# Performance work log

Hardware: AMD Instinct MI355X
Metric: run time of the kernel (lower is better)

## Reference

```python
import jax, jax.numpy as jnp
import numpy as np

HIDDEN = 1024
NHEAD = 16
HEAD_DIM = HIDDEN // NHEAD
B, S = 2, 2048


def setup_inputs() -> dict:
    key = jax.random.key(0)
    ks = jax.random.split(key, 10)
    scale = 1.0 / np.sqrt(HIDDEN)
    inp = {
        "x": jax.random.normal(ks[0], (B, S, HIDDEN), dtype=jnp.float32),
        "mask": jax.random.randint(ks[1], (B, S), 0, 2).astype(bool),
        "Wq": jax.random.normal(ks[2], (HIDDEN, HIDDEN), dtype=jnp.float32) * scale,
        "bq": jnp.zeros((HIDDEN,), dtype=jnp.float32),
        "Wk": jax.random.normal(ks[3], (HIDDEN, HIDDEN), dtype=jnp.float32) * scale,
        "bk": jnp.zeros((HIDDEN,), dtype=jnp.float32),
        "Wv": jax.random.normal(ks[4], (HIDDEN, HIDDEN), dtype=jnp.float32) * scale,
        "bv": jnp.zeros((HIDDEN,), dtype=jnp.float32),
        "Wo": jax.random.normal(ks[5], (HIDDEN, HIDDEN), dtype=jnp.float32) * scale,
        "bo": jnp.zeros((HIDDEN,), dtype=jnp.float32),
    }
    return inp


def reference(x, mask, Wq, bq, Wk, bk, Wv, bv, Wo, bo):
    B_, S_, H = x.shape
    # QKV projections (torch Linear: x @ W.T + b), split into heads -> [B, nhead, S, head_dim]
    def split_heads(t):
        return t.reshape(B_, S_, NHEAD, HEAD_DIM).transpose(0, 2, 1, 3)

    q = split_heads(x @ Wq.T + bq)
    k = split_heads(x @ Wk.T + bk)
    v = split_heads(x @ Wv.T + bv)

    # scaled dot-product scores: [B, nhead, S, S]
    energy = jnp.einsum("bhqd,bhkd->bhqk", q, k) / jnp.sqrt(jnp.float32(HEAD_DIM))

    # combined padding + diagonal-exclusion mask: mask keys where mask[b,k] is True,
    # but never mask the diagonal (self) position
    eye = jnp.eye(S_, dtype=bool)  # [S, S]
    attn_mask = mask[:, None, None, :] & ~eye[None, None, :, :]  # [B, 1, S, S] broadcast over heads
    energy = jnp.where(attn_mask, -jnp.inf, energy)

    attention = jax.nn.softmax(energy, axis=-1)
    out = jnp.einsum("bhqk,bhkd->bhqd", attention, v)  # [B, nhead, S, head_dim]
    out = out.transpose(0, 2, 1, 3).reshape(B_, S_, H)
    return out @ Wo.T + bo
```

## Files before the change

### kernel.cpp

```cpp
#include <hip/hip_runtime.h>

typedef __attribute__((ext_vector_type(8))) short short8;
typedef __attribute__((ext_vector_type(4))) float f32x4;
typedef __attribute__((ext_vector_type(16))) float f32x16;
typedef __attribute__((ext_vector_type(4))) unsigned short ushort4v;

#define HIDDEN 1024
#define NHEAD 16
#define HD 64
#define BATCH 2
#define SEQ 2048
#define MROWS (BATCH * SEQ)
#define QSCALE 0.18033688011112042f

__device__ __forceinline__ unsigned short f2b(float f) {
  union { float f; unsigned u; } v; v.f = f;
  unsigned r = v.u + 0x7fffu + ((v.u >> 16) & 1u);
  return (unsigned short)(r >> 16);
}

__device__ __forceinline__ unsigned cvt_pk_bf16(float lo, float hi) {
  unsigned r;
  asm("v_cvt_pk_bf16_f32 %0, %1, %2" : "=v"(r) : "v"(lo), "v"(hi));
  return r;
}

__device__ __forceinline__ float fexp2(float x) {
#if __has_builtin(__builtin_amdgcn_exp2f)
  return __builtin_amdgcn_exp2f(x);
#else
  return exp2f(x);
#endif
}

__device__ __forceinline__ void gll16(const void* g, void* l) {
  __builtin_amdgcn_global_load_lds(
      (__attribute__((address_space(1))) void*)g,
      (__attribute__((address_space(3))) void*)l, 16, 0, 0);
}

__global__ void prep_kernel(const float* __restrict__ x,
                            const float* __restrict__ Wq,
                            const float* __restrict__ Wk,
                            const float* __restrict__ Wv,
                            const float* __restrict__ Wo,
                            unsigned short* __restrict__ xb,
                            unsigned short* __restrict__ wqb,
                            unsigned short* __restrict__ wkb,
                            unsigned short* __restrict__ wvb,
                            unsigned short* __restrict__ wob) {
  int bid = blockIdx.x;
  const float* src;
  unsigned short* dst;
  int base;
  if (bid < 4096)      { src = x;  dst = xb;  base = bid; }
  else if (bid < 5120) { src = Wq; dst = wqb; base = bid - 4096; }
  else if (bid < 6144) { src = Wk; dst = wkb; base = bid - 5120; }
  else if (bid < 7168) { src = Wv; dst = wvb; base = bid - 6144; }
  else                 { src = Wo; dst = wob; base = bid - 7168; }
  int i = (base * 256 + threadIdx.x) * 4;
  float4 v = *reinterpret_cast<const float4*>(src + i);
  ushort4v o;
  o.x = f2b(v.x); o.y = f2b(v.y); o.z = f2b(v.z); o.w = f2b(v.w);
  *reinterpret_cast<ushort4v*>(dst + i) = o;
}

__global__ void amask_kernel(const int* __restrict__ m, float* __restrict__ am,
                             int n) {
  int i = blockIdx.x * blockDim.x + threadIdx.x;
  if (i < n) am[i] = m[i] ? -1e30f : 0.f;
}

template <int MODE>
__global__ __launch_bounds__(256) void gemm128_kernel(
    const unsigned short* __restrict__ A,
    const unsigned short* __restrict__ W0,
    const unsigned short* __restrict__ W1,
    const unsigned short* __restrict__ W2,
    const float* __restrict__ c0, const float* __restrict__ c1,
    const float* __restrict__ c2, void* __restrict__ o0,
    void* __restrict__ o1, void* __restrict__ o2) {
  __shared__ __align__(16) unsigned short Al[2][128 * 64];
  __shared__ __align__(16) unsigned short Bl[2][128 * 64];
  const int t = threadIdx.x;
  const int w = t >> 6, l = t & 63;
  const int hi = l >> 4, lo16 = l & 15;
  const int wr = w >> 1, wc = w & 1;
  const int m0 = blockIdx.x * 128;
  const int n0 = blockIdx.y * 128;
  const int K = HIDDEN;

  const unsigned short* Bsel;
  const float* bias;
  int region = 0, n_loc = n0;
  if (MODE == 0) {
    region = n0 >> 10;
    n_loc = n0 & 1023;
    Bsel = region == 0 ? W0 : (region == 1 ? W1 : W2);
    bias = region == 0 ? c0 : (region == 1 ? c1 : c2);
  } else {
    Bsel = W0;
    bias = c0;
  }

  const int srow = w * 32 + (l >> 3);
  const int schunk = (l & 7) ^ (l >> 3);
  const int rsw = (lo16 & 7);

  const unsigned short* pA[4];
  const unsigned short* pB[4];
#pragma unroll
  for (int i = 0; i < 4; ++i) {
    pA[i] = A + (size_t)(m0 + srow + i * 8) * K + schunk * 8;
    pB[i] = Bsel + (size_t)(n_loc + srow + i * 8) * K + schunk * 8;
  }

  f32x4 acc[4][4];
#pragma unroll
  for (int mi = 0; mi < 4; ++mi)
#pragma unroll
    for (int f = 0; f < 4; ++f) acc[mi][f] = f32x4{0.f, 0.f, 0.f, 0.f};

#pragma unroll
  for (int i = 0; i < 4; ++i) {
    gll16(pA[i], &Al[0][(w * 32 + i * 8) * 64]);
    gll16(pB[i], &Bl[0][(w * 32 + i * 8) * 64]);
    pA[i] += 64; pB[i] += 64;
  }
  __syncthreads();

  auto step = [&](int knext, int BUF) __attribute__((always_inline)) {
    if (knext < K) {
#pragma unroll
      for (int i = 0; i < 4; ++i) {
        gll16(pA[i], &Al[BUF ^ 1][(w * 32 + i * 8) * 64]);
        gll16(pB[i], &Bl[BUF ^ 1][(w * 32 + i * 8) * 64]);
        pA[i] += 64; pB[i] += 64;
      }
    }
#pragma unroll
    for (int kk = 0; kk < 2; ++kk) {
      short8 af[4], bf[4];
#pragma unroll
      for (int mi = 0; mi < 4; ++mi) {
        int row = wr * 64 + mi * 16 + lo16;
        af[mi] = *reinterpret_cast<const short8*>(
            &Al[BUF][row * 64 + (((kk * 4 + hi) ^ rsw) * 8)]);
      }
#pragma unroll
      for (int f = 0; f < 4; ++f) {
        int row = wc * 64 + f * 16 + lo16;
        bf[f] = *reinterpret_cast<const short8*>(
            &Bl[BUF][row * 64 + (((kk * 4 + hi) ^ rsw) * 8)]);
      }
#pragma unroll
      for (int mi = 0; mi < 4; ++mi)
#pragma unroll
        for (int f = 0; f < 4; ++f)
          acc[mi][f] =
              __builtin_amdgcn_mfma_f32_16x16x32_bf16(af[mi], bf[f], acc[mi][f], 0, 0, 0);
    }
    __syncthreads();
  };

  for (int kt = 0; kt < K; kt += 128) {
    step(kt + 64, 0);
    step(kt + 128, 1);
  }

#pragma unroll
  for (int mi = 0; mi < 4; ++mi)
#pragma unroll
    for (int f = 0; f < 4; ++f) {
      int mbase = m0 + wr * 64 + mi * 16 + hi * 4;
      int n_rel = n_loc + wc * 64 + f * 16 + lo16;
      float bv_ = bias[n_rel];
      if (MODE == 0 && region == 2) {
        int b = mbase >> 11, s = mbase & 2047, d = n_rel & 63, h = n_rel >> 6;
        uint2 pk;
        pk.x = cvt_pk_bf16(acc[mi][f][0] + bv_, acc[mi][f][1] + bv_);
        pk.y = cvt_pk_bf16(acc[mi][f][2] + bv_, acc[mi][f][3] + bv_);
        *reinterpret_cast<uint2*>(
            (unsigned short*)o2 + ((size_t)(b * NHEAD + h) * HD + d) * SEQ + s) = pk;
        continue;
      }
#pragma unroll
      for (int j = 0; j < 4; ++j) {
        float v = acc[mi][f][j] + bv_;
        int mm = mbase + j;
        if (MODE == 0) {
          int b = mm >> 11, s = mm & 2047, h = n_rel >> 6, d = n_rel & 63;
          if (region == 0)
            ((unsigned short*)o0)[((size_t)(b * NHEAD + h) * SEQ + s) * HD + d] =
                f2b(v * QSCALE);
          else
            ((unsigned short*)o1)[((size_t)(b * NHEAD + h) * SEQ + s) * HD + d] =
                f2b(v);
        } else {
          ((float*)o0)[(size_t)mm * HIDDEN + n_rel] = v;
        }
      }
    }
}

__global__ __launch_bounds__(512) void attn_kernel(
    const unsigned short* __restrict__ Q, const unsigned short* __restrict__ Km,
    const unsigned short* __restrict__ Vt, const float* __restrict__ amf,
    unsigned short* __restrict__ O) {
  __shared__ __align__(16) unsigned short KV[2][2][64 * 64];
  __shared__ float SrwS[4][64];
  const int t = threadIdx.x;
  const int w = t >> 6, l = t & 63;
  const int q31 = l & 31, hi32 = l >> 5;
  const int qg = w >> 1, half = w & 1;
  const int bh = blockIdx.y;
  const int b = bh >> 4, h = bh & 15;
  const int q0w = blockIdx.x * 128 + qg * 32;
  const int q = q0w + q31;
  const bool diagw = (half == (qg & 1));
  const int dtile = blockIdx.x * 128 + (qg >> 1) * 64;

  const unsigned short* Qb = Q + (size_t)bh * SEQ * HD;
  const unsigned short* Kb = Km + (size_t)bh * SEQ * HD;
  const unsigned short* Vb = Vt + (size_t)bh * HD * SEQ;
  const float* mb = amf + b * SEQ + half * 32;

  short8 qf[4];
#pragma unroll
  for (int dc = 0; dc < 4; ++dc)
    qf[dc] = *reinterpret_cast<const short8*>(
        Qb + (size_t)q * HD + dc * 16 + hi32 * 8);

  f32x16 o0, o1;
#pragma unroll
  for (int r = 0; r < 16; ++r) { o0[r] = 0.f; o1[r] = 0.f; }
  float srw = 0.f;

  const int srow = w * 8 + (l >> 3);
  const int sc_ = ((l & 7) ^ (l >> 3) ^ (w & 3)) * 8;
  const unsigned short* pK = Kb + (size_t)srow * HD + sc_;
  const unsigned short* pV = Vb + (size_t)srow * SEQ + sc_;

  gll16(pK, &KV[0][0][(w * 8) * 64]);
  gll16(pV, &KV[0][1][(w * 8) * 64]);
  pK += 64 * HD; pV += 64;
  __syncthreads();

  const int rk = (q31 & 7) ^ (q31 >> 3);

  auto step = [&](int k0, int BUF) __attribute__((always_inline)) {
    float4 a0[4];
#pragma unroll
    for (int g = 0; g < 4; ++g)
      a0[g] = *reinterpret_cast<const float4*>(mb + k0 + g * 8 + hi32 * 4);

    if (k0 + 64 < SEQ) {
      gll16(pK, &KV[BUF ^ 1][0][(w * 8) * 64]);
      gll16(pV, &KV[BUF ^ 1][1][(w * 8) * 64]);
      pK += 64 * HD; pV += 64;
    }

    f32x16 s0;
    if (diagw && k0 == dtile) {
      int kb = hi32 * 4;
#pragma unroll
      for (int g = 0; g < 4; ++g) {
        if (kb + g * 8 + 0 == q31) a0[g].x = 0.f;
        if (kb + g * 8 + 1 == q31) a0[g].y = 0.f;
        if (kb + g * 8 + 2 == q31) a0[g].z = 0.f;
        if (kb + g * 8 + 3 == q31) a0[g].w = 0.f;
      }
    }
#pragma unroll
    for (int g = 0; g < 4; ++g) {
      s0[4 * g + 0] = a0[g].x; s0[4 * g + 1] = a0[g].y;
      s0[4 * g + 2] = a0[g].z; s0[4 * g + 3] = a0[g].w;
    }

    __builtin_amdgcn_s_setprio(1);
#pragma unroll
    for (int dc = 0; dc < 4; ++dc) {
      short8 kf = *reinterpret_cast<const short8*>(
          &KV[BUF][0][(half * 32 + q31) * 64 + (((dc * 2 + hi32) ^ rk) * 8)]);
      s0 = __builtin_amdgcn_mfma_f32_32x32x16_bf16(kf, qf[dc], s0, 0, 0, 0);
    }
    __builtin_amdgcn_s_setprio(0);

    float sum = 0.f;
#pragma unroll
    for (int r = 0; r < 16; ++r) {
      float p = fexp2(s0[r]);
      s0[r] = p;
      sum += p;
    }
    {
      unsigned a = __float_as_uint(sum), bsw = a;
      auto rr = __builtin_amdgcn_permlane32_swap(a, bsw, false, false);
      sum = __uint_as_float(rr[0]) + __uint_as_float(rr[1]);
    }
    srw += sum;

    unsigned c[8];
#pragma unroll
    for (int R = 0; R < 4; ++R) {
      c[R * 2 + 0] = cvt_pk_bf16(s0[4 * R + 0], s0[4 * R + 1]);
      c[R * 2 + 1] = cvt_pk_bf16(s0[4 * R + 2], s0[4 * R + 3]);
    }

    short8 pb[2];
#pragma unroll
    for (int sl = 0; sl < 2; ++sl) {
      const int R0 = sl * 2;
      auto r0 = __builtin_amdgcn_permlane32_swap(c[R0 * 2 + 0],
                                                 c[(R0 + 1) * 2 + 0], false, false);
      auto r1 = __builtin_amdgcn_permlane32_swap(c[R0 * 2 + 1],
                                                 c[(R0 + 1) * 2 + 1], false, false);
      union { unsigned u[4]; short8 s8; } pu;
      pu.u[0] = r0[0]; pu.u[1] = r1[0]; pu.u[2] = r0[1]; pu.u[3] = r1[1];
      pb[sl] = pu.s8;
    }

    __builtin_amdgcn_s_setprio(1);
#pragma unroll
    for (int sl = 0; sl < 2; ++sl) {
      int ch = (((half * 2 + sl) * 2 + hi32) ^ rk) * 8;
      short8 vf0 = *reinterpret_cast<const short8*>(&KV[BUF][1][q31 * 64 + ch]);
      short8 vf1 =
          *reinterpret_cast<const short8*>(&KV[BUF][1][(32 + q31) * 64 + ch]);
      o0 = __builtin_amdgcn_mfma_f32_32x32x16_bf16(vf0, pb[sl], o0, 0, 0, 0);
      o1 = __builtin_amdgcn_mfma_f32_32x32x16_bf16(vf1, pb[sl], o1, 0, 0, 0);
    }
    __builtin_amdgcn_s_setprio(0);

    __syncthreads();
  };

  for (int k0 = 0; k0 < SEQ; k0 += 128) {
    step(k0, 0);
    step(k0 + 64, 1);
  }

  float* obuf = (float*)&KV[0][0][0];
  if (half) {
    float* d = obuf + (qg * 64 + l) * 32;
#pragma unroll
    for (int r = 0; r < 16; ++r) { d[r] = o0[r]; d[16 + r] = o1[r]; }
    SrwS[qg][l] = srw;
  }
  __syncthreads();
  if (!half) {
    const float* d = obuf + (qg * 64 + l) * 32;
#pragma unroll
    for (int r = 0; r < 16; ++r) { o0[r] += d[r]; o1[r] += d[16 + r]; }
    srw += SrwS[qg][l];

    float rinv = 1.f / srw;
    unsigned short* Ob = O + (size_t)(b * SEQ + q) * HIDDEN + h * HD;
#pragma unroll
    for (int g = 0; g < 4; ++g) {
      uint2 w0, w1;
      w0.x = cvt_pk_bf16(o0[4 * g + 0] * rinv, o0[4 * g + 1] * rinv);
      w0.y = cvt_pk_bf16(o0[4 * g + 2] * rinv, o0[4 * g + 3] * rinv);
      w1.x = cvt_pk_bf16(o1[4 * g + 0] * rinv, o1[4 * g + 1] * rinv);
      w1.y = cvt_pk_bf16(o1[4 * g + 2] * rinv, o1[4 * g + 3] * rinv);
      *reinterpret_cast<uint2*>(Ob + 8 * g + 4 * hi32) = w0;
      *reinterpret_cast<uint2*>(Ob + 32 + 8 * g + 4 * hi32) = w1;
    }
  }
}

extern "C" void kernel_launch(void* const* d_in, const int* in_sizes, int n_in,
                              void* d_out, int out_size, void* d_ws,
                              size_t ws_size, hipStream_t stream) {
  const float* x = (const float*)d_in[0];
  const int* mask = (const int*)d_in[1];
  const float* Wq = (const float*)d_in[2];
  const float* bq = (const float*)d_in[3];
  const float* Wk = (const float*)d_in[4];
  const float* bk = (const float*)d_in[5];
  const float* Wv = (const float*)d_in[6];
  const float* bv = (const float*)d_in[7];
  const float* Wo = (const float*)d_in[8];
  const float* bo = (const float*)d_in[9];

  char* ws = (char*)d_ws;
  unsigned short* xb  = (unsigned short*)(ws + ((size_t)0 << 20));
  unsigned short* wqb = (unsigned short*)(ws + ((size_t)8 << 20));
  unsigned short* wkb = (unsigned short*)(ws + ((size_t)10 << 20));
  unsigned short* wvb = (unsigned short*)(ws + ((size_t)12 << 20));
  unsigned short* wob = (unsigned short*)(ws + ((size_t)14 << 20));
  unsigned short* qw  = (unsigned short*)(ws + ((size_t)16 << 20));
  unsigned short* kw  = (unsigned short*)(ws + ((size_t)24 << 20));
  unsigned short* vtw = (unsigned short*)(ws + ((size_t)32 << 20));
  unsigned short* ow  = (unsigned short*)(ws + ((size_t)40 << 20));
  float* amf = (float*)(ws + ((size_t)0 << 20));

  prep_kernel<<<8192, 256, 0, stream>>>(x, Wq, Wk, Wv, Wo, xb, wqb, wkb, wvb,
                                        wob);

  gemm128_kernel<0><<<dim3(MROWS / 128, 3 * HIDDEN / 128), 256, 0, stream>>>(
      xb, wqb, wkb, wvb, bq, bk, bv, qw, kw, vtw);

  amask_kernel<<<MROWS / 256, 256, 0, stream>>>(mask, amf, MROWS);

  attn_kernel<<<dim3(SEQ / 128, BATCH * NHEAD), 512, 0, stream>>>(qw, kw, vtw,
                                                                  amf, ow);

  gemm128_kernel<1><<<dim3(MROWS / 128, HIDDEN / 128), 256, 0, stream>>>(
      ow, wob, nullptr, nullptr, bo, nullptr, nullptr, d_out, nullptr, nullptr);
}
```

Baseline: 128.9 us.

## Double KV tile to 128 keys per barrier and remap blocks across XCDs

The attention kernel now stages 128-key K and V tiles per buffer instead of 64, so each wave processes two 32-key sub-blocks between barriers. This halves the number of __syncthreads and load-issue rounds. The grid becomes 1D with a block-index permutation that spreads blocks across the chiplets (XCDs), and the output reduction buffer stride is padded to 33 to avoid LDS bank conflicts. The cost is twice the LDS per block, which may lower occupancy, plus a new swizzle scheme for V.

```diff
diff --git a/kernel.cpp b/kernel.cpp
--- a/kernel.cpp
+++ b/kernel.cpp
@@ -207,23 +207,25 @@
     const unsigned short* __restrict__ Q, const unsigned short* __restrict__ Km,
     const unsigned short* __restrict__ Vt, const float* __restrict__ amf,
     unsigned short* __restrict__ O) {
-  __shared__ __align__(16) unsigned short KV[2][2][64 * 64];
+  __shared__ __align__(16) unsigned short SMEM[2 * (128 * 64 + 64 * 128)];
   __shared__ float SrwS[4][64];
+#define KL(B) (&SMEM[(B) * (128 * 64 + 64 * 128)])
+#define VL(B) (KL(B) + 128 * 64)
   const int t = threadIdx.x;
   const int w = t >> 6, l = t & 63;
   const int q31 = l & 31, hi32 = l >> 5;
   const int qg = w >> 1, half = w & 1;
-  const int bh = blockIdx.y;
+  const int nb = ((blockIdx.x & 7) << 6) | (blockIdx.x >> 3);
+  const int qt = nb & 15, bh = nb >> 4;
   const int b = bh >> 4, h = bh & 15;
-  const int q0w = blockIdx.x * 128 + qg * 32;
+  const int q0w = qt * 128 + qg * 32;
   const int q = q0w + q31;
-  const bool diagw = (half == (qg & 1));
-  const int dtile = blockIdx.x * 128 + (qg >> 1) * 64;
+  const int dtile = qt * 128;
 
   const unsigned short* Qb = Q + (size_t)bh * SEQ * HD;
   const unsigned short* Kb = Km + (size_t)bh * SEQ * HD;
   const unsigned short* Vb = Vt + (size_t)bh * HD * SEQ;
-  const float* mb = amf + b * SEQ + half * 32;
+  const float* mb = amf + b * SEQ;
 
   short8 qf[4];
 #pragma unroll
@@ -236,41 +238,59 @@
   for (int r = 0; r < 16; ++r) { o0[r] = 0.f; o1[r] = 0.f; }
   float srw = 0.f;
 
-  const int srow = w * 8 + (l >> 3);
-  const int sc_ = ((l & 7) ^ (l >> 3) ^ (w & 3)) * 8;
-  const unsigned short* pK = Kb + (size_t)srow * HD + sc_;
-  const unsigned short* pV = Vb + (size_t)srow * SEQ + sc_;
-
-  gll16(pK, &KV[0][0][(w * 8) * 64]);
-  gll16(pV, &KV[0][1][(w * 8) * 64]);
-  pK += 64 * HD; pV += 64;
+  const unsigned short* pK[2];
+#pragma unroll
+  for (int i = 0; i < 2; ++i) {
+    int row = w * 16 + i * 8 + (l >> 3);
+    int sc = ((l & 7) ^ (l >> 3) ^ ((w * 2 + i) & 3)) * 8;
+    pK[i] = Kb + (size_t)row * HD + sc;
+  }
+  const unsigned short* pV[2];
+#pragma unroll
+  for (int i = 0; i < 2; ++i) {
+    int row = w * 8 + i * 4 + (l >> 4);
+    int c = l & 15;
+    int key = (row & 7) ^ ((row >> 3) & 3);
+    int sc = (c & 8) | ((c & 7) ^ key);
+    pV[i] = Vb + (size_t)row * SEQ + sc * 8;
+  }
+
+  auto stage = [&](int BUF) __attribute__((always_inline)) {
+#pragma unroll
+    for (int i = 0; i < 2; ++i) {
+      gll16(pK[i], KL(BUF) + (w * 16 + i * 8) * 64);
+      pK[i] += 128 * HD;
+    }
+#pragma unroll
+    for (int i = 0; i < 2; ++i) {
+      gll16(pV[i], VL(BUF) + (w * 8 + i * 4) * 128);
+      pV[i] += 128;
+    }
+  };
+
+  stage(0);
   __syncthreads();
 
   const int rk = (q31 & 7) ^ (q31 >> 3);
 
-  auto step = [&](int k0, int BUF) __attribute__((always_inline)) {
+  auto sub = [&](int k0, int kb, int BUF) __attribute__((always_inline)) {
+    const float* mb2 = mb + k0 + half * 64 + kb * 32;
     float4 a0[4];
 #pragma unroll
     for (int g = 0; g < 4; ++g)
-      a0[g] = *reinterpret_cast<const float4*>(mb + k0 + g * 8 + hi32 * 4);
-
-    if (k0 + 64 < SEQ) {
-      gll16(pK, &KV[BUF ^ 1][0][(w * 8) * 64]);
-      gll16(pV, &KV[BUF ^ 1][1][(w * 8) * 64]);
-      pK += 64 * HD; pV += 64;
-    }
-
+      a0[g] = *reinterpret_cast<const float4*>(mb2 + g * 8 + hi32 * 4);
+
+    if (k0 == dtile && qg == 2 * half + kb) {
+      int kbq = hi32 * 4;
+#pragma unroll
+      for (int g = 0; g < 4; ++g) {
+        if (kbq + g * 8 + 0 == q31) a0[g].x = 0.f;
+        if (kbq + g * 8 + 1 == q31) a0[g].y = 0.f;
+        if (kbq + g * 8 + 2 == q31) a0[g].z = 0.f;
+        if (kbq + g * 8 + 3 == q31) a0[g].w = 0.f;
+      }
+    }
     f32x16 s0;
-    if (diagw && k0 == dtile) {
-      int kb = hi32 * 4;
-#pragma unroll
-      for (int g = 0; g < 4; ++g) {
-        if (kb + g * 8 + 0 == q31) a0[g].x = 0.f;
-        if (kb + g * 8 + 1 == q31) a0[g].y = 0.f;
-        if (kb + g * 8 + 2 == q31) a0[g].z = 0.f;
-        if (kb + g * 8 + 3 == q31) a0[g].w = 0.f;
-      }
-    }
 #pragma unroll
     for (int g = 0; g < 4; ++g) {
       s0[4 * g + 0] = a0[g].x; s0[4 * g + 1] = a0[g].y;
@@ -281,7 +301,7 @@
 #pragma unroll
     for (int dc = 0; dc < 4; ++dc) {
       short8 kf = *reinterpret_cast<const short8*>(
-          &KV[BUF][0][(half * 32 + q31) * 64 + (((dc * 2 + hi32) ^ rk) * 8)]);
+          KL(BUF) + (half * 64 + kb * 32 + q31) * 64 + (((dc * 2 + hi32) ^ rk) * 8));
       s0 = __builtin_amdgcn_mfma_f32_32x32x16_bf16(kf, qf[dc], s0, 0, 0, 0);
     }
     __builtin_amdgcn_s_setprio(0);
@@ -323,33 +343,39 @@
     __builtin_amdgcn_s_setprio(1);
 #pragma unroll
     for (int sl = 0; sl < 2; ++sl) {
-      int ch = (((half * 2 + sl) * 2 + hi32) ^ rk) * 8;
-      short8 vf0 = *reinterpret_cast<const short8*>(&KV[BUF][1][q31 * 64 + ch]);
+      int chunk = half * 8 + kb * 4 + sl * 2 + hi32;
+      int ch = ((chunk & 8) | ((chunk & 7) ^ rk)) * 8;
+      short8 vf0 = *reinterpret_cast<const short8*>(VL(BUF) + q31 * 128 + ch);
       short8 vf1 =
-          *reinterpret_cast<const short8*>(&KV[BUF][1][(32 + q31) * 64 + ch]);
+          *reinterpret_cast<const short8*>(VL(BUF) + (32 + q31) * 128 + ch);
       o0 = __builtin_amdgcn_mfma_f32_32x32x16_bf16(vf0, pb[sl], o0, 0, 0, 0);
       o1 = __builtin_amdgcn_mfma_f32_32x32x16_bf16(vf1, pb[sl], o1, 0, 0, 0);
     }
     __builtin_amdgcn_s_setprio(0);
-
+  };
+
+  auto step = [&](int k0, int BUF) __attribute__((always_inline)) {
+    if (k0 + 128 < SEQ) stage(BUF ^ 1);
+    sub(k0, 0, BUF);
+    sub(k0, 1, BUF);
     __syncthreads();
   };
 
-  for (int k0 = 0; k0 < SEQ; k0 += 128) {
+  for (int k0 = 0; k0 < SEQ; k0 += 256) {
     step(k0, 0);
-    step(k0 + 64, 1);
-  }
-
-  float* obuf = (float*)&KV[0][0][0];
+    step(k0 + 128, 1);
+  }
+
+  float* obuf = (float*)SMEM;
   if (half) {
-    float* d = obuf + (qg * 64 + l) * 32;
+    float* d = obuf + (qg * 64 + l) * 33;
 #pragma unroll
     for (int r = 0; r < 16; ++r) { d[r] = o0[r]; d[16 + r] = o1[r]; }
     SrwS[qg][l] = srw;
   }
   __syncthreads();
   if (!half) {
-    const float* d = obuf + (qg * 64 + l) * 32;
+    const float* d = obuf + (qg * 64 + l) * 33;
 #pragma unroll
     for (int r = 0; r < 16; ++r) { o0[r] += d[r]; o1[r] += d[16 + r]; }
     srw += SrwS[qg][l];
@@ -367,6 +393,8 @@
       *reinterpret_cast<uint2*>(Ob + 32 + 8 * g + 4 * hi32) = w1;
     }
   }
+#undef KL
+#undef VL
 }
 
 extern "C" void kernel_launch(void* const* d_in, const int* in_sizes, int n_in,
@@ -403,8 +431,7 @@
 
   amask_kernel<<<MROWS / 256, 256, 0, stream>>>(mask, amf, MROWS);
 
-  attn_kernel<<<dim3(SEQ / 128, BATCH * NHEAD), 512, 0, stream>>>(qw, kw, vtw,
-                                                                  amf, ow);
+  attn_kernel<<<512, 512, 0, stream>>>(qw, kw, vtw, amf, ow);
 
   gemm128_kernel<1><<<dim3(MROWS / 128, HIDDEN / 128), 256, 0, stream>>>(
       ow, wob, nullptr, nullptr, bo, nullptr, nullptr, d_out, nullptr, nullptr);
```

After: 127.8 us. About the same (-0.8%).
